# Optimization experiments

Measured on AMD Instinct MI355X. Metric: run time of the kernel, lower is better.

## Reference

```python
import jax, jax.numpy as jnp
import numpy as np

B, N, H, O = 262144, 64, 256, 64
MAX_ITER = 30
TOL = 1e-7
NU = 1.0


def setup_inputs() -> dict:
    key = jax.random.key(0)
    kx, kr, k1, k2, k3, k4 = jax.random.split(key, 6)
    x = jax.random.normal(kx, (B, N), dtype=jnp.float32) * 3.0
    r = jax.random.uniform(kr, (N,), dtype=jnp.float32) + 0.5  # positive rates in [0.5, 1.5)
    # MLP params (torch Linear: y = x @ W.T + b), Kaiming-ish scaling
    W1 = jax.random.normal(k1, (H, N), dtype=jnp.float32) * (1.0 / np.sqrt(N))
    b1 = jax.random.normal(k2, (H,), dtype=jnp.float32) * 0.01
    W2 = jax.random.normal(k3, (O, H), dtype=jnp.float32) * (1.0 / np.sqrt(H))
    b2 = jax.random.normal(k4, (O,), dtype=jnp.float32) * 0.01
    return {"x": x, "r": r, "W1": W1, "b1": b1, "W2": W2, "b2": b2}


def _solve_s(x, r):
    """Vectorized Newton solve of sum_i e^{-2 r_i s} x_i^2 = 1 per sample.

    Replicates solve_s_single: s starts at 0, up to MAX_ITER Newton steps,
    frozen once |F(s)| < TOL; all-zero samples return s = 0.
    """
    x2 = x * x  # [B, N]
    zero_mask = jnp.all(jnp.abs(x) <= 1e-12, axis=1)  # torch.allclose(x, 0, atol=1e-12)

    def body(_, s):
        e = jnp.exp(-2.0 * r[None, :] * s[:, None])        # [B, N]
        val = jnp.sum(e * x2, axis=1) - 1.0                # F(s)     [B]
        dval = jnp.sum(-2.0 * r[None, :] * e * x2, axis=1) # F'(s)    [B]
        safe_d = jnp.where(dval == 0.0, 1.0, dval)
        step = val / safe_d
        step = jnp.where((jnp.abs(val) < TOL) | zero_mask, 0.0, step)
        return s - step

    s0 = jnp.zeros(x.shape[0], dtype=x.dtype)
    return jax.lax.fori_loop(0, MAX_ITER, body, s0)


def reference(x, r, W1, b1, W2, b2):
    S = _solve_s(x, r)[:, None]                 # [B, 1], detached in torch (built via .item())
    S = jax.lax.stop_gradient(S)
    x_sphere = x * jnp.exp(-r[None, :] * S)     # d(-s) x
    h = jnp.maximum(x_sphere @ W1.T + b1, 0.0)  # [B, H]
    mlp_out = h @ W2.T + b2                     # [B, O]
    return mlp_out * jnp.exp(NU * S)
```

## Files before the change

kernel.cpp:

```cpp
#include <hip/hip_runtime.h>

typedef __attribute__((ext_vector_type(8))) short short8;
typedef __attribute__((ext_vector_type(4))) float floatx4;

static __device__ __forceinline__ unsigned short f2bf(float f) {
    unsigned u = __float_as_uint(f);
    u += 0x7FFFu + ((u >> 16) & 1u);
    return (unsigned short)(u >> 16);
}

__global__ __launch_bounds__(256) void convert_w_k(const float* __restrict__ W1,
                                                   const float* __restrict__ W2,
                                                   unsigned short* __restrict__ w1b,
                                                   unsigned short* __restrict__ w2b) {
    int i = blockIdx.x * 256 + threadIdx.x;
    w1b[i] = f2bf(W1[i]);
    w2b[i] = f2bf(W2[i]);
}

__global__ __launch_bounds__(256) void newton_k(const float* __restrict__ x,
                                                const float* __restrict__ r,
                                                unsigned short* __restrict__ xs,
                                                float* __restrict__ scl) {
    int tid = blockIdx.x * 256 + threadIdx.x;
    int sample = tid >> 2;
    int part = tid & 3;

    const float4* x4 = (const float4*)(x + (size_t)sample * 64 + part * 16);
    const float4* r4 = (const float4*)(r + part * 16);
    const float L2E2 = 2.8853900817779268f;
    float xv[16], rl2[16], x2[16], rx2[16];
#pragma unroll
    for (int j = 0; j < 4; ++j) {
        float4 a = x4[j];
        float4 b = r4[j];
        xv[4 * j + 0] = a.x; xv[4 * j + 1] = a.y; xv[4 * j + 2] = a.z; xv[4 * j + 3] = a.w;
        float r0 = b.x, r1 = b.y, r2 = b.z, r3 = b.w;
        rl2[4 * j + 0] = r0 * L2E2; rl2[4 * j + 1] = r1 * L2E2;
        rl2[4 * j + 2] = r2 * L2E2; rl2[4 * j + 3] = r3 * L2E2;
        float q0 = a.x * a.x, q1 = a.y * a.y, q2 = a.z * a.z, q3 = a.w * a.w;
        x2[4 * j + 0] = q0; x2[4 * j + 1] = q1; x2[4 * j + 2] = q2; x2[4 * j + 3] = q3;
        rx2[4 * j + 0] = r0 * q0; rx2[4 * j + 1] = r1 * q1;
        rx2[4 * j + 2] = r2 * q2; rx2[4 * j + 3] = r3 * q3;
    }

    float sum0 = 0.f, sumr = 0.f;
    int nz = 0;
#pragma unroll
    for (int j = 0; j < 16; ++j) {
        sum0 += x2[j];
        sumr += rx2[j];
        nz |= (fabsf(xv[j]) > 1e-12f) ? 1 : 0;
    }
    sum0 += __shfl_xor(sum0, 1); sum0 += __shfl_xor(sum0, 2);
    sumr += __shfl_xor(sumr, 1); sumr += __shfl_xor(sumr, 2);
    nz   |= __shfl_xor(nz, 1);   nz   |= __shfl_xor(nz, 2);

    float s = 0.f;
    if (nz) {
        s = __logf(sum0) * sum0 * __builtin_amdgcn_rcpf(2.f * sumr);
#pragma unroll 1
        for (int it = 0; it < 10; ++it) {
            float ns = -s;
            float v = 0.f, dv = 0.f;
#pragma unroll
            for (int j = 0; j < 16; ++j) {
                float e = __builtin_amdgcn_exp2f(ns * rl2[j]);
                v = fmaf(e, x2[j], v);
                dv = fmaf(e, rx2[j], dv);
            }
            v += __shfl_xor(v, 1);   v += __shfl_xor(v, 2);
            dv += __shfl_xor(dv, 1); dv += __shfl_xor(dv, 2);
            if (__all(fabsf(v - 1.f) < 1e-5f)) break;
            s += __logf(v) * v * __builtin_amdgcn_rcpf(2.f * dv);
        }
    }

    float hs = -0.5f * s;
    unsigned up[8];
#pragma unroll
    for (int j = 0; j < 8; ++j) {
        float a = xv[2 * j] * __builtin_amdgcn_exp2f(hs * rl2[2 * j]);
        float b = xv[2 * j + 1] * __builtin_amdgcn_exp2f(hs * rl2[2 * j + 1]);
        up[j] = (unsigned)f2bf(a) | ((unsigned)f2bf(b) << 16);
    }
    uint4* dst = (uint4*)(xs + (size_t)sample * 64 + part * 16);
    dst[0] = make_uint4(up[0], up[1], up[2], up[3]);
    dst[1] = make_uint4(up[4], up[5], up[6], up[7]);
    if (part == 0) scl[sample] = __expf(s);
}

__global__ __launch_bounds__(256, 2) void mlp_k(const unsigned short* __restrict__ xs,
                                                const float* __restrict__ scl,
                                                const unsigned short* __restrict__ w1b,
                                                const unsigned short* __restrict__ w2b,
                                                const float* __restrict__ b1,
                                                const float* __restrict__ b2,
                                                float* __restrict__ out,
                                                int tiles_per_block) {
    __shared__ unsigned short sW1[256 * 64];
    __shared__ unsigned short sW2[64 * 256];
    __shared__ unsigned short sH[64 * 64];

    int tid = threadIdx.x;

    const uint4* w1u = (const uint4*)w1b;
#pragma unroll
    for (int c = 0; c < 8; ++c) {
        int g = tid + c * 256;
        int row = g >> 3, ch = g & 7;
        *(uint4*)&sW1[row * 64 + (ch ^ (row & 7)) * 8] = w1u[g];
    }
    const uint4* w2u = (const uint4*)w2b;
#pragma unroll
    for (int c = 0; c < 8; ++c) {
        int g = tid + c * 256;
        int row = g >> 5, ch = g & 31;
        *(uint4*)&sW2[row * 256 + (ch ^ (row & 7)) * 8] = w2u[g];
    }
    __syncthreads();

    int wave = tid >> 6, lane = tid & 63;
    int q = lane >> 4, l16 = lane & 15;
    int sx = l16 & 7;

    float bias1[16];
#pragma unroll
    for (int n = 0; n < 16; ++n) bias1[n] = b1[n * 16 + l16];
    float bias2[4];
#pragma unroll
    for (int n = 0; n < 4; ++n) bias2[n] = b2[n * 16 + l16];

    for (int tt = 0; tt < tiles_per_block; ++tt) {
        size_t m0 = ((size_t)blockIdx.x * tiles_per_block + tt) * 64;
        int myrow = wave * 16 + l16;

        const short8* xrow = (const short8*)(xs + (m0 + myrow) * 64);
        short8 a0 = xrow[q];
        short8 a1 = xrow[q + 4];
        float sc[4];
#pragma unroll
        for (int reg = 0; reg < 4; ++reg) sc[reg] = scl[m0 + wave * 16 + q * 4 + reg];

        floatx4 oacc[4];
#pragma unroll
        for (int n = 0; n < 4; ++n) oacc[n] = (floatx4){0.f, 0.f, 0.f, 0.f};

#pragma unroll
        for (int hc = 0; hc < 4; ++hc) {
#pragma unroll
            for (int n = 0; n < 4; ++n) {
                int hcol = hc * 4 + n;
                int row = hcol * 16 + l16;
                short8 wb0 = *(const short8*)&sW1[row * 64 + (q ^ sx) * 8];
                short8 wb1 = *(const short8*)&sW1[row * 64 + ((q + 4) ^ sx) * 8];
                floatx4 acc = {0.f, 0.f, 0.f, 0.f};
                acc = __builtin_amdgcn_mfma_f32_16x16x32_bf16(a0, wb0, acc, 0, 0, 0);
                acc = __builtin_amdgcn_mfma_f32_16x16x32_bf16(a1, wb1, acc, 0, 0, 0);
                float bias = bias1[hcol];
#pragma unroll
                for (int reg = 0; reg < 4; ++reg) {
                    float h = acc[reg] + bias;
                    h = h > 0.f ? h : 0.f;
                    int rr = wave * 16 + q * 4 + reg;
                    int E = n * 16 + l16;
                    sH[rr * 64 + (((E >> 3) ^ (rr & 7)) * 8) + (E & 7)] = f2bf(h);
                }
            }
            short8 ha0 = *(const short8*)&sH[myrow * 64 + (q ^ sx) * 8];
            short8 ha1 = *(const short8*)&sH[myrow * 64 + ((q + 4) ^ sx) * 8];
#pragma unroll
            for (int n = 0; n < 4; ++n) {
                int row = n * 16 + l16;
                short8 wb0 = *(const short8*)&sW2[row * 256 + (hc * 8 + (q ^ sx)) * 8];
                short8 wb1 = *(const short8*)&sW2[row * 256 + (hc * 8 + ((q + 4) ^ sx)) * 8];
                oacc[n] = __builtin_amdgcn_mfma_f32_16x16x32_bf16(ha0, wb0, oacc[n], 0, 0, 0);
                oacc[n] = __builtin_amdgcn_mfma_f32_16x16x32_bf16(ha1, wb1, oacc[n], 0, 0, 0);
            }
        }
#pragma unroll
        for (int n = 0; n < 4; ++n) {
#pragma unroll
            for (int reg = 0; reg < 4; ++reg) {
                float o = (oacc[n][reg] + bias2[n]) * sc[reg];
                out[(m0 + wave * 16 + q * 4 + reg) * 64 + n * 16 + l16] = o;
            }
        }
    }
}

extern "C" void kernel_launch(void* const* d_in, const int* in_sizes, int n_in,
                              void* d_out, int out_size, void* d_ws, size_t ws_size,
                              hipStream_t stream) {
    const float* x  = (const float*)d_in[0];
    const float* r  = (const float*)d_in[1];
    const float* W1 = (const float*)d_in[2];
    const float* b1 = (const float*)d_in[3];
    const float* W2 = (const float*)d_in[4];
    const float* b2 = (const float*)d_in[5];
    float* out = (float*)d_out;
    int B = in_sizes[0] / 64;

    char* ws = (char*)d_ws;
    unsigned short* w1b = (unsigned short*)ws;
    unsigned short* w2b = (unsigned short*)(ws + 32768);
    float* scl = (float*)(ws + 65536);
    unsigned short* xs = (unsigned short*)(ws + 65536 + (size_t)B * 4);

    convert_w_k<<<64, 256, 0, stream>>>(W1, W2, w1b, w2b);
    newton_k<<<B / 64, 256, 0, stream>>>(x, r, xs, scl);

    int tiles = B / 64;
    int blocks = 512;
    int tpb = tiles / blocks;
    mlp_k<<<blocks, 256, 0, stream>>>(xs, scl, w1b, w2b, b1, b2, out, tpb);
}
```

Measured before the change: 146.6 us.

## Fuse weight conversion, Newton solve and MLP into one kernel

Merges the three kernels into one. Each block converts the fp32 weights to bf16 straight into shared memory, and each wave runs the per-sample Newton solve in the lanes that already hold the MFMA A-operand rows. This removes the round trip of the bf16 scaled-x and scale buffers through global memory and two kernel launches. The cost is redundant weight conversion in every block and Newton work sitting on the MLP kernel's critical path, at an occupancy limited by shared memory and registers.

```diff
diff --git a/kernel.cpp b/kernel.cpp
--- a/kernel.cpp
+++ b/kernel.cpp
@@ -9,114 +9,45 @@
     return (unsigned short)(u >> 16);
 }
 
-__global__ __launch_bounds__(256) void convert_w_k(const float* __restrict__ W1,
-                                                   const float* __restrict__ W2,
-                                                   unsigned short* __restrict__ w1b,
-                                                   unsigned short* __restrict__ w2b) {
-    int i = blockIdx.x * 256 + threadIdx.x;
-    w1b[i] = f2bf(W1[i]);
-    w2b[i] = f2bf(W2[i]);
-}
-
-__global__ __launch_bounds__(256) void newton_k(const float* __restrict__ x,
-                                                const float* __restrict__ r,
-                                                unsigned short* __restrict__ xs,
-                                                float* __restrict__ scl) {
-    int tid = blockIdx.x * 256 + threadIdx.x;
-    int sample = tid >> 2;
-    int part = tid & 3;
-
-    const float4* x4 = (const float4*)(x + (size_t)sample * 64 + part * 16);
-    const float4* r4 = (const float4*)(r + part * 16);
-    const float L2E2 = 2.8853900817779268f;
-    float xv[16], rl2[16], x2[16], rx2[16];
-#pragma unroll
-    for (int j = 0; j < 4; ++j) {
-        float4 a = x4[j];
-        float4 b = r4[j];
-        xv[4 * j + 0] = a.x; xv[4 * j + 1] = a.y; xv[4 * j + 2] = a.z; xv[4 * j + 3] = a.w;
-        float r0 = b.x, r1 = b.y, r2 = b.z, r3 = b.w;
-        rl2[4 * j + 0] = r0 * L2E2; rl2[4 * j + 1] = r1 * L2E2;
-        rl2[4 * j + 2] = r2 * L2E2; rl2[4 * j + 3] = r3 * L2E2;
-        float q0 = a.x * a.x, q1 = a.y * a.y, q2 = a.z * a.z, q3 = a.w * a.w;
-        x2[4 * j + 0] = q0; x2[4 * j + 1] = q1; x2[4 * j + 2] = q2; x2[4 * j + 3] = q3;
-        rx2[4 * j + 0] = r0 * q0; rx2[4 * j + 1] = r1 * q1;
-        rx2[4 * j + 2] = r2 * q2; rx2[4 * j + 3] = r3 * q3;
-    }
-
-    float sum0 = 0.f, sumr = 0.f;
-    int nz = 0;
-#pragma unroll
-    for (int j = 0; j < 16; ++j) {
-        sum0 += x2[j];
-        sumr += rx2[j];
-        nz |= (fabsf(xv[j]) > 1e-12f) ? 1 : 0;
-    }
-    sum0 += __shfl_xor(sum0, 1); sum0 += __shfl_xor(sum0, 2);
-    sumr += __shfl_xor(sumr, 1); sumr += __shfl_xor(sumr, 2);
-    nz   |= __shfl_xor(nz, 1);   nz   |= __shfl_xor(nz, 2);
-
-    float s = 0.f;
-    if (nz) {
-        s = __logf(sum0) * sum0 * __builtin_amdgcn_rcpf(2.f * sumr);
-#pragma unroll 1
-        for (int it = 0; it < 10; ++it) {
-            float ns = -s;
-            float v = 0.f, dv = 0.f;
-#pragma unroll
-            for (int j = 0; j < 16; ++j) {
-                float e = __builtin_amdgcn_exp2f(ns * rl2[j]);
-                v = fmaf(e, x2[j], v);
-                dv = fmaf(e, rx2[j], dv);
-            }
-            v += __shfl_xor(v, 1);   v += __shfl_xor(v, 2);
-            dv += __shfl_xor(dv, 1); dv += __shfl_xor(dv, 2);
-            if (__all(fabsf(v - 1.f) < 1e-5f)) break;
-            s += __logf(v) * v * __builtin_amdgcn_rcpf(2.f * dv);
-        }
-    }
-
-    float hs = -0.5f * s;
-    unsigned up[8];
-#pragma unroll
-    for (int j = 0; j < 8; ++j) {
-        float a = xv[2 * j] * __builtin_amdgcn_exp2f(hs * rl2[2 * j]);
-        float b = xv[2 * j + 1] * __builtin_amdgcn_exp2f(hs * rl2[2 * j + 1]);
-        up[j] = (unsigned)f2bf(a) | ((unsigned)f2bf(b) << 16);
-    }
-    uint4* dst = (uint4*)(xs + (size_t)sample * 64 + part * 16);
-    dst[0] = make_uint4(up[0], up[1], up[2], up[3]);
-    dst[1] = make_uint4(up[4], up[5], up[6], up[7]);
-    if (part == 0) scl[sample] = __expf(s);
-}
-
-__global__ __launch_bounds__(256, 2) void mlp_k(const unsigned short* __restrict__ xs,
-                                                const float* __restrict__ scl,
-                                                const unsigned short* __restrict__ w1b,
-                                                const unsigned short* __restrict__ w2b,
-                                                const float* __restrict__ b1,
-                                                const float* __restrict__ b2,
-                                                float* __restrict__ out,
-                                                int tiles_per_block) {
+__global__ __launch_bounds__(256, 2) void fused_k(const float* __restrict__ x,
+                                                  const float* __restrict__ r,
+                                                  const float* __restrict__ W1f,
+                                                  const float* __restrict__ b1,
+                                                  const float* __restrict__ W2f,
+                                                  const float* __restrict__ b2,
+                                                  float* __restrict__ out,
+                                                  int tiles_per_block) {
     __shared__ unsigned short sW1[256 * 64];
     __shared__ unsigned short sW2[64 * 256];
     __shared__ unsigned short sH[64 * 64];
 
     int tid = threadIdx.x;
 
-    const uint4* w1u = (const uint4*)w1b;
+    const float4* w1f4 = (const float4*)W1f;
 #pragma unroll
     for (int c = 0; c < 8; ++c) {
         int g = tid + c * 256;
+        float4 lo = w1f4[2 * g], hi = w1f4[2 * g + 1];
+        uint4 p;
+        p.x = (unsigned)f2bf(lo.x) | ((unsigned)f2bf(lo.y) << 16);
+        p.y = (unsigned)f2bf(lo.z) | ((unsigned)f2bf(lo.w) << 16);
+        p.z = (unsigned)f2bf(hi.x) | ((unsigned)f2bf(hi.y) << 16);
+        p.w = (unsigned)f2bf(hi.z) | ((unsigned)f2bf(hi.w) << 16);
         int row = g >> 3, ch = g & 7;
-        *(uint4*)&sW1[row * 64 + (ch ^ (row & 7)) * 8] = w1u[g];
-    }
-    const uint4* w2u = (const uint4*)w2b;
+        *(uint4*)&sW1[row * 64 + (ch ^ (row & 7)) * 8] = p;
+    }
+    const float4* w2f4 = (const float4*)W2f;
 #pragma unroll
     for (int c = 0; c < 8; ++c) {
         int g = tid + c * 256;
+        float4 lo = w2f4[2 * g], hi = w2f4[2 * g + 1];
+        uint4 p;
+        p.x = (unsigned)f2bf(lo.x) | ((unsigned)f2bf(lo.y) << 16);
+        p.y = (unsigned)f2bf(lo.z) | ((unsigned)f2bf(lo.w) << 16);
+        p.z = (unsigned)f2bf(hi.x) | ((unsigned)f2bf(hi.y) << 16);
+        p.w = (unsigned)f2bf(hi.z) | ((unsigned)f2bf(hi.w) << 16);
         int row = g >> 5, ch = g & 31;
-        *(uint4*)&sW2[row * 256 + (ch ^ (row & 7)) * 8] = w2u[g];
+        *(uint4*)&sW2[row * 256 + (ch ^ (row & 7)) * 8] = p;
     }
     __syncthreads();
 
@@ -131,16 +62,79 @@
 #pragma unroll
     for (int n = 0; n < 4; ++n) bias2[n] = b2[n * 16 + l16];
 
+    const float L2E2 = 2.8853900817779268f;
+    float rl2[16];
+    {
+        const float4* r4 = (const float4*)r;
+        float4 ra = r4[2 * q], rb = r4[2 * q + 1];
+        float4 rc = r4[8 + 2 * q], rd = r4[8 + 2 * q + 1];
+        rl2[0] = ra.x * L2E2; rl2[1] = ra.y * L2E2; rl2[2] = ra.z * L2E2; rl2[3] = ra.w * L2E2;
+        rl2[4] = rb.x * L2E2; rl2[5] = rb.y * L2E2; rl2[6] = rb.z * L2E2; rl2[7] = rb.w * L2E2;
+        rl2[8] = rc.x * L2E2; rl2[9] = rc.y * L2E2; rl2[10] = rc.z * L2E2; rl2[11] = rc.w * L2E2;
+        rl2[12] = rd.x * L2E2; rl2[13] = rd.y * L2E2; rl2[14] = rd.z * L2E2; rl2[15] = rd.w * L2E2;
+    }
+
     for (int tt = 0; tt < tiles_per_block; ++tt) {
         size_t m0 = ((size_t)blockIdx.x * tiles_per_block + tt) * 64;
         int myrow = wave * 16 + l16;
 
-        const short8* xrow = (const short8*)(xs + (m0 + myrow) * 64);
-        short8 a0 = xrow[q];
-        short8 a1 = xrow[q + 4];
+        const float4* x4 = (const float4*)(x + (m0 + myrow) * 64);
+        float4 va = x4[2 * q], vb = x4[2 * q + 1];
+        float4 vc = x4[8 + 2 * q], vd = x4[8 + 2 * q + 1];
+        float xv[16];
+        xv[0] = va.x; xv[1] = va.y; xv[2] = va.z; xv[3] = va.w;
+        xv[4] = vb.x; xv[5] = vb.y; xv[6] = vb.z; xv[7] = vb.w;
+        xv[8] = vc.x; xv[9] = vc.y; xv[10] = vc.z; xv[11] = vc.w;
+        xv[12] = vd.x; xv[13] = vd.y; xv[14] = vd.z; xv[15] = vd.w;
+
+        float x2[16], rx2[16];
+        float sum0 = 0.f, sumr = 0.f;
+        int nz = 0;
+#pragma unroll
+        for (int j = 0; j < 16; ++j) {
+            x2[j] = xv[j] * xv[j];
+            rx2[j] = rl2[j] * x2[j];
+            sum0 += x2[j];
+            sumr += rx2[j];
+            nz |= (fabsf(xv[j]) > 1e-12f) ? 1 : 0;
+        }
+        sum0 += __shfl_xor(sum0, 16); sum0 += __shfl_xor(sum0, 32);
+        sumr += __shfl_xor(sumr, 16); sumr += __shfl_xor(sumr, 32);
+        nz   |= __shfl_xor(nz, 16);   nz   |= __shfl_xor(nz, 32);
+
+        float s = 0.f;
+        if (nz) {
+            s = __log2f(sum0) * sum0 * __builtin_amdgcn_rcpf(sumr);
+#pragma unroll 1
+            for (int it = 0; it < 10; ++it) {
+                float ns = -s;
+                float v = 0.f, dv = 0.f;
+#pragma unroll
+                for (int j = 0; j < 16; ++j) {
+                    float e = __builtin_amdgcn_exp2f(ns * rl2[j]);
+                    v = fmaf(e, x2[j], v);
+                    dv = fmaf(e, rx2[j], dv);
+                }
+                v += __shfl_xor(v, 16);   v += __shfl_xor(v, 32);
+                dv += __shfl_xor(dv, 16); dv += __shfl_xor(dv, 32);
+                if (__all(fabsf(v - 1.f) < 1e-5f)) break;
+                s += __log2f(v) * v * __builtin_amdgcn_rcpf(dv);
+            }
+        }
+
+        float hs = -0.5f * s;
+        short8 a0, a1;
+#pragma unroll
+        for (int j = 0; j < 8; ++j)
+            a0[j] = (short)f2bf(xv[j] * __builtin_amdgcn_exp2f(hs * rl2[j]));
+#pragma unroll
+        for (int j = 0; j < 8; ++j)
+            a1[j] = (short)f2bf(xv[8 + j] * __builtin_amdgcn_exp2f(hs * rl2[8 + j]));
+
+        float es = __builtin_amdgcn_exp2f(s * 1.4426950408889634f);
         float sc[4];
 #pragma unroll
-        for (int reg = 0; reg < 4; ++reg) sc[reg] = scl[m0 + wave * 16 + q * 4 + reg];
+        for (int reg = 0; reg < 4; ++reg) sc[reg] = __shfl(es, q * 4 + reg);
 
         floatx4 oacc[4];
 #pragma unroll
@@ -201,17 +195,9 @@
     float* out = (float*)d_out;
     int B = in_sizes[0] / 64;
 
-    char* ws = (char*)d_ws;
-    unsigned short* w1b = (unsigned short*)ws;
-    unsigned short* w2b = (unsigned short*)(ws + 32768);
-    float* scl = (float*)(ws + 65536);
-    unsigned short* xs = (unsigned short*)(ws + 65536 + (size_t)B * 4);
-
-    convert_w_k<<<64, 256, 0, stream>>>(W1, W2, w1b, w2b);
-    newton_k<<<B / 64, 256, 0, stream>>>(x, r, xs, scl);
-
     int tiles = B / 64;
     int blocks = 512;
     int tpb = tiles / blocks;
-    mlp_k<<<blocks, 256, 0, stream>>>(xs, scl, w1b, w2b, b1, b2, out, tpb);
+
+    fused_k<<<blocks, 256, 0, stream>>>(x, r, W1, b1, W2, b2, out, tpb);
 }
```

Result: no change. 144.3 us (-1.6%).
